# Optimization experiments

Measured on AMD Instinct MI355X. Metric: run time of the kernel, lower is better.

The kernel has to match this reference:

```python
import jax, jax.numpy as jnp
import numpy as np

D_MODEL = 1024
N_HEADS = 16
N_KV_HEADS = 4
HEAD_DIM = 64


def setup_inputs() -> dict:
    key = jax.random.key(0)
    ks = jax.random.split(key, 5)
    B, T, P = 2, 512, 8
    scale = 1.0 / np.sqrt(D_MODEL)
    return {
        "hidden_states": jax.random.normal(ks[0], (B, T, P, D_MODEL), dtype=jnp.float32),
        # weights stored [in, out] so y = x @ W (same math as nn.Linear with W^T)
        "Wq": jax.random.normal(ks[1], (D_MODEL, N_HEADS * HEAD_DIM), dtype=jnp.float32) * scale,
        "Wk": jax.random.normal(ks[2], (D_MODEL, N_KV_HEADS * HEAD_DIM), dtype=jnp.float32) * scale,
        "Wv": jax.random.normal(ks[3], (D_MODEL, N_KV_HEADS * HEAD_DIM), dtype=jnp.float32) * scale,
        "Wo": jax.random.normal(ks[4], (N_HEADS * HEAD_DIM, D_MODEL), dtype=jnp.float32) * scale,
    }


def _rope_tables(T, d):
    half = d // 2
    inv_freq = 1.0 / (10000.0 ** (jnp.arange(half, dtype=jnp.float32) / half))
    pos = jnp.arange(T, dtype=jnp.float32)
    angles = pos[:, None] * inv_freq[None, :]  # (T, half)
    return jnp.cos(angles), jnp.sin(angles)


def _apply_rope(x, cos, sin):
    # x: (B, P, T, H, d); cos/sin: (T, d/2)
    half = x.shape[-1] // 2
    x1, x2 = x[..., :half], x[..., half:]
    c = cos[None, None, :, None, :]
    s = sin[None, None, :, None, :]
    return jnp.concatenate([x1 * c - x2 * s, x1 * s + x2 * c], axis=-1)


def reference(hidden_states, Wq, Wk, Wv, Wo):
    B, T, P, _ = hidden_states.shape
    x = jnp.transpose(hidden_states, (0, 2, 1, 3))  # (B, P, T, C)
    q = (x @ Wq).reshape(B, P, T, N_HEADS, HEAD_DIM)
    k = (x @ Wk).reshape(B, P, T, N_KV_HEADS, HEAD_DIM)
    v = (x @ Wv).reshape(B, P, T, N_KV_HEADS, HEAD_DIM)

    rep = N_HEADS // N_KV_HEADS
    k = jnp.repeat(k, rep, axis=3)  # (B,P,T,H,d) interleaved like torch repeat/view
    v = jnp.repeat(v, rep, axis=3)

    cos, sin = _rope_tables(T, HEAD_DIM)
    q = _apply_rope(q, cos, sin)
    k = _apply_rope(k, cos, sin)

    # (B,P,H,T,d)
    q = jnp.transpose(q, (0, 1, 3, 2, 4))
    k = jnp.transpose(k, (0, 1, 3, 2, 4))
    v = jnp.transpose(v, (0, 1, 3, 2, 4))

    attn = jnp.einsum("bphqd,bphkd->bphqk", q, k) / jnp.sqrt(
        jnp.asarray(HEAD_DIM, q.dtype))
    attn = jax.nn.softmax(attn, axis=-1)
    out = jnp.einsum("bphqk,bphkd->bphqd", attn, v)
    out = jnp.transpose(out, (0, 1, 3, 2, 4)).reshape(B, P, T, N_HEADS * HEAD_DIM)
    out = jnp.transpose(out, (0, 2, 1, 3))  # (B, T, P, H*d)
    return out @ Wo
```

## Files before the change

### kernel.cpp

```cpp
#include <hip/hip_runtime.h>
#include <stdint.h>


typedef __attribute__((ext_vector_type(8))) short bf16x8;
typedef __attribute__((ext_vector_type(4))) float f32x4;
typedef __attribute__((ext_vector_type(16))) float f32x16;
typedef __attribute__((ext_vector_type(4))) unsigned short us4;
typedef __attribute__((ext_vector_type(8))) unsigned short us8;

static __device__ __forceinline__ unsigned short f2bf(float f) {
  unsigned u = __float_as_uint(f);
  u += 0x7fffu + ((u >> 16) & 1u);
  return (unsigned short)(u >> 16);
}

static __device__ __forceinline__ void ld_lds16(const void* g, void* l) {
  __builtin_amdgcn_global_load_lds(
      (const __attribute__((address_space(1))) void*)g,
      (__attribute__((address_space(3))) void*)l, 16, 0, 0);
}

static __device__ __forceinline__ f32x4 mfma16(bf16x8 a, bf16x8 b, f32x4 c) {
  return __builtin_amdgcn_mfma_f32_16x16x32_bf16(a, b, c, 0, 0, 0);
}
static __device__ __forceinline__ f32x16 mfma32(bf16x8 a, bf16x8 b, f32x16 c) {
  return __builtin_amdgcn_mfma_f32_32x32x16_bf16(a, b, c, 0, 0, 0);
}

__global__ __launch_bounds__(256) void conv_all(
    const float* __restrict__ hs, const float* __restrict__ Wq,
    const float* __restrict__ Wk, const float* __restrict__ Wv,
    const float* __restrict__ Wo, unsigned short* __restrict__ xb,
    unsigned short* __restrict__ wqkv, unsigned short* __restrict__ wot) {
  __shared__ float tile[64][65];
  int bid = blockIdx.x, tid = threadIdx.x;
  if (bid < 8192) {
    int gid = bid * 256 + tid;
    size_t e = (size_t)gid * 4;
    int r = (int)(e >> 10);
    int d = (int)(e & 1023);
    int b = r >> 12, p = (r >> 9) & 7, t = r & 511;
    const float4* src = (const float4*)(hs + ((((size_t)b * 512 + t) * 8 + p) << 10) + d);
    float4 v = *src;
    us4 o;
    o.x = f2bf(v.x); o.y = f2bf(v.y); o.z = f2bf(v.z); o.w = f2bf(v.w);
    *(us4*)(xb + e) = o;
    return;
  }
  int tb = bid - 8192;
  const float* W; unsigned short* Wt; int N, tc0, tn0;
  if (tb < 256)      { W = Wq; Wt = wqkv;                       N = 1024; tc0 = (tb >> 4) * 64;          tn0 = (tb & 15) * 64; }
  else if (tb < 320) { W = Wk; Wt = wqkv + (size_t)1024 * 1024; N = 256;  tc0 = ((tb - 256) >> 2) * 64;  tn0 = ((tb - 256) & 3) * 64; }
  else if (tb < 384) { W = Wv; Wt = wqkv + (size_t)1280 * 1024; N = 256;  tc0 = ((tb - 320) >> 2) * 64;  tn0 = ((tb - 320) & 3) * 64; }
  else               { W = Wo; Wt = wot;                        N = 1024; tc0 = ((tb - 384) >> 4) * 64;  tn0 = ((tb - 384) & 15) * 64; }
  int tr = tid >> 4, tc = tid & 15;
#pragma unroll
  for (int i = 0; i < 4; ++i) {
    int c = tr + i * 16;
    float4 v = *(const float4*)(W + (size_t)(tc0 + c) * N + tn0 + tc * 4);
    tile[c][tc * 4 + 0] = v.x; tile[c][tc * 4 + 1] = v.y;
    tile[c][tc * 4 + 2] = v.z; tile[c][tc * 4 + 3] = v.w;
  }
  __syncthreads();
#pragma unroll
  for (int i = 0; i < 4; ++i) {
    int n = tr + i * 16;
    us4 o;
    o.x = f2bf(tile[tc * 4 + 0][n]); o.y = f2bf(tile[tc * 4 + 1][n]);
    o.z = f2bf(tile[tc * 4 + 2][n]); o.w = f2bf(tile[tc * 4 + 3][n]);
    *(us4*)(Wt + (size_t)(tn0 + n) * 1024 + tc0 + tc * 4) = o;
  }
}

template <int NT, int MODE>
__global__ __launch_bounds__(256, 3) void gemm_bt(
    const unsigned short* __restrict__ A, const unsigned short* __restrict__ Bt,
    unsigned short* __restrict__ qb, unsigned short* __restrict__ kb,
    unsigned short* __restrict__ vtb, float* __restrict__ out) {
  constexpr int K = 1024;
  __shared__ __align__(16) unsigned short Sm[128 * 128];
  unsigned short* As = Sm;
  unsigned short* Bs = Sm + 128 * 64;
  unsigned short* Cs = Sm;

  int tid = threadIdx.x;
  int lane = tid & 63, wid = tid >> 6;
  int quad = lane >> 4, lo = lane & 15;
  int tn = blockIdx.x % NT, tm = blockIdx.x / NT;
  int wm = (wid >> 1) * 64, wn = (wid & 1) * 64;
  int srow = lane >> 3, schunk = lane & 7;

  f32x4 z = {0.f, 0.f, 0.f, 0.f};
  f32x4 acc[4][4];
  for (int i = 0; i < 4; ++i) for (int j = 0; j < 4; ++j) acc[i][j] = z;

  int cg = schunk ^ srow;
  const unsigned short* pa = A + ((size_t)(tm * 128) + wid * 8 + srow) * K + cg * 8;
  const unsigned short* pb = Bt + ((size_t)(tn * 128) + wid * 8 + srow) * K + cg * 8;
  char* dA = (char*)As + (wid * 8) * 128;
  char* dB = (char*)Bs + (wid * 8) * 128;

  for (int k0 = 0; k0 < K; k0 += 64) {
    __syncthreads();
#pragma unroll
    for (int i = 0; i < 4; ++i) {
      ld_lds16(pa + (size_t)i * 32 * K + k0, dA + i * 32 * 128);
      ld_lds16(pb + (size_t)i * 32 * K + k0, dB + i * 32 * 128);
    }
    __syncthreads();
#pragma unroll
    for (int kk = 0; kk < 64; kk += 32) {
      bf16x8 af[4], bb[4];
#pragma unroll
      for (int mi = 0; mi < 4; ++mi) {
        int row = wm + mi * 16 + lo;
        int cgx = (quad + (kk >> 3)) ^ (row & 7);
        af[mi] = *(const bf16x8*)(As + (size_t)row * 64 + cgx * 8);
      }
#pragma unroll
      for (int ni = 0; ni < 4; ++ni) {
        int row = wn + ni * 16 + lo;
        int cgx = (quad + (kk >> 3)) ^ (row & 7);
        bb[ni] = *(const bf16x8*)(Bs + (size_t)row * 64 + cgx * 8);
      }
#pragma unroll
      for (int mi = 0; mi < 4; ++mi)
#pragma unroll
        for (int ni = 0; ni < 4; ++ni)
          acc[mi][ni] = mfma16(af[mi], bb[ni], acc[mi][ni]);
    }
  }

  __syncthreads();

  if (MODE == 0 && tn < 10) {
    float qscale = (tn < 8) ? 0.125f : 1.0f;
#pragma unroll
    for (int mi = 0; mi < 4; ++mi)
#pragma unroll
      for (int r = 0; r < 4; ++r) {
        int t = (tm * 128 + wm + mi * 16 + quad * 4 + r) & 511;
#pragma unroll
        for (int ni = 0; ni < 2; ++ni) {
          float inv = exp2f((float)(ni * 16 + lo) * -0.41524101186092029f);
          float ang = (float)t * inv;
          float s, c;
          __sincosf(ang, &s, &c);
          float x1 = acc[mi][ni][r], x2 = acc[mi][ni + 2][r];
          acc[mi][ni][r]     = (x1 * c - x2 * s) * qscale;
          acc[mi][ni + 2][r] = (x1 * s + x2 * c) * qscale;
        }
      }
#pragma unroll
    for (int mi = 0; mi < 4; ++mi)
#pragma unroll
      for (int ni = 0; ni < 4; ++ni)
#pragma unroll
        for (int r = 0; r < 4; ++r) {
          int row = wm + mi * 16 + quad * 4 + r;
          int col = wn + ni * 16 + lo;
          int cs = col ^ (((row >> 2) & 3) << 3);
          Cs[row * 128 + cs] = f2bf(acc[mi][ni][r]);
        }
    __syncthreads();
    int tc = tid & 15, ro = tid >> 4;
#pragma unroll
    for (int it = 0; it < 8; ++it) {
      int row = ro + 16 * it;
      int cs = (tc * 8) ^ (((row >> 2) & 3) << 3);
      us8 v = *(const us8*)(Cs + row * 128 + cs);
      size_t grow = (size_t)(tm * 128 + row);
      if (tn < 8) {
        *(us8*)(qb + grow * 1024 + tn * 128 + tc * 8) = v;
      } else {
        *(us8*)(kb + grow * 256 + (tn - 8) * 128 + tc * 8) = v;
      }
    }
  } else if (MODE == 0) {
#pragma unroll
    for (int mi = 0; mi < 4; ++mi)
#pragma unroll
      for (int ni = 0; ni < 4; ++ni)
#pragma unroll
        for (int r = 0; r < 4; ++r) {
          int trow = wm + mi * 16 + quad * 4 + r;
          int col = wn + ni * 16 + lo;
          Cs[col * 128 + (trow ^ ((col & 7) << 3))] = f2bf(acc[mi][ni][r]);
        }
    __syncthreads();
    int chunk = tid & 15, colIdx = tid >> 4;
    int bp = tm >> 2, tbase = (tm & 3) * 128;
#pragma unroll
    for (int it = 0; it < 8; ++it) {
      int col = colIdx + it * 16;
      int t0 = chunk * 8;
      us8 v = *(const us8*)(Cs + col * 128 + (t0 ^ ((col & 7) << 3)));
      int gc = (tn - 10) * 128 + col;
      int hh = gc >> 6, dd = gc & 63;
      *(us8*)(vtb + (((size_t)(bp * 4 + hh)) * 64 + dd) * 512 + tbase + t0) = v;
    }
  } else {
    for (int mi = 0; mi < 4; ++mi) {
      for (int ni = 0; ni < 4; ++ni) {
        int col = tn * 128 + wn + ni * 16 + lo;
        for (int r = 0; r < 4; ++r) {
          int grow = tm * 128 + wm + mi * 16 + quad * 4 + r;
          int bp = grow >> 9, t = grow & 511;
          int b = bp >> 3, p = bp & 7;
          out[((((size_t)b * 512 + t) * 8 + p) << 10) + col] = acc[mi][ni][r];
        }
      }
    }
  }
}

__global__ __launch_bounds__(256, 4) void attn(
    const unsigned short* __restrict__ qb, const unsigned short* __restrict__ kb,
    const unsigned short* __restrict__ vtb, unsigned short* __restrict__ ao) {
  __shared__ __align__(16) unsigned short Qs[128 * 64];
  __shared__ __align__(16) unsigned short Ks[64 * 64];
  __shared__ __align__(16) unsigned short Vs[64 * 64];

  int tid = threadIdx.x;
  int lane = tid & 63, wid = tid >> 6;
  int lo32 = lane & 31, hl = lane >> 5;
  int qt = blockIdx.x & 3, bph = blockIdx.x >> 2;
  int head = bph & 15, bp = bph >> 4;
  int kvh = head >> 2;
  int t0 = qt * 128;
  int srow = lane >> 3, schunk = lane & 7;

  const unsigned short* qg = qb + ((size_t)(bp * 512 + t0)) * 1024 + head * 64;
  const unsigned short* kg = kb + ((size_t)bp * 512) * 256 + kvh * 64;
  const unsigned short* vg = vtb + ((size_t)(bp * 4 + kvh)) * 64 * 512;

  for (int i = 0; i < 4; ++i) {
    int row = wid * 8 + i * 32 + srow;
    int cg = schunk ^ (row & 7);
    ld_lds16(qg + (size_t)row * 1024 + cg * 8, (char*)Qs + (wid * 8 + i * 32) * 128);
  }

  f32x16 z16 = {0.f};
  f32x16 o0 = z16, o1 = z16;
  float psum = 0.f;
  int qrow = wid * 32 + lo32;

  for (int kt = 0; kt < 512; kt += 64) {
    __syncthreads();
    for (int i = 0; i < 2; ++i) {
      int row = wid * 8 + i * 32 + srow;
      int cg = schunk ^ (row & 7);
      ld_lds16(kg + (size_t)(kt + row) * 256 + cg * 8, (char*)Ks + (wid * 8 + i * 32) * 128);
      ld_lds16(vg + (size_t)row * 512 + kt + cg * 8, (char*)Vs + (wid * 8 + i * 32) * 128);
    }
    __syncthreads();

    f32x16 st0 = z16, st1 = z16;
#pragma unroll
    for (int kkc = 0; kkc < 4; ++kkc) {
      int ch = 2 * kkc + hl;
      bf16x8 qf = *(const bf16x8*)(Qs + (size_t)qrow * 64 + ((ch ^ (qrow & 7)) * 8));
      bf16x8 kf0 = *(const bf16x8*)(Ks + (size_t)lo32 * 64 + ((ch ^ (lo32 & 7)) * 8));
      bf16x8 kf1 = *(const bf16x8*)(Ks + (size_t)(32 + lo32) * 64 + ((ch ^ (lo32 & 7)) * 8));
      st0 = mfma32(kf0, qf, st0);
      st1 = mfma32(kf1, qf, st1);
    }

#pragma unroll
    for (int t = 0; t < 2; ++t) {
      const f32x16& stv = t ? st1 : st0;
      unsigned pk[8], xpk[8];
#pragma unroll
      for (int p = 0; p < 8; ++p) {
        float e0 = __expf(stv[2 * p]);
        float e1 = __expf(stv[2 * p + 1]);
        psum += e0 + e1;
        pk[p] = ((__float_as_uint(e0) + 0x8000u) >> 16) |
                ((__float_as_uint(e1) + 0x8000u) & 0xffff0000u);
      }
#pragma unroll
      for (int p = 0; p < 8; ++p) xpk[p] = (unsigned)__shfl_xor((int)pk[p], 32);
#pragma unroll
      for (int cc = 0; cc < 2; ++cc) {
        int o = cc * 4;
        union { unsigned u[4]; bf16x8 v; } af;
        if (hl == 0) {
          af.u[0] = pk[o];      af.u[1] = pk[o + 1];
          af.u[2] = xpk[o];     af.u[3] = xpk[o + 1];
        } else {
          af.u[0] = xpk[o + 2]; af.u[1] = xpk[o + 3];
          af.u[2] = pk[o + 2];  af.u[3] = pk[o + 3];
        }
        int vch = 2 * (t * 2 + cc) + hl;
        bf16x8 v0 = *(const bf16x8*)(Vs + (size_t)lo32 * 64 + ((vch ^ (lo32 & 7)) * 8));
        bf16x8 v1 = *(const bf16x8*)(Vs + (size_t)(32 + lo32) * 64 + ((vch ^ (lo32 & 7)) * 8));
        o0 = mfma32(af.v, v0, o0);
        o1 = mfma32(af.v, v1, o1);
      }
    }
  }

  psum += __shfl_xor(psum, 32);
  float inv = 1.f / psum;
#pragma unroll
  for (int r = 0; r < 16; ++r) {
    int q_r = (r & 3) + 8 * (r >> 2) + 4 * hl;
    float sc = __shfl(inv, q_r);
    size_t grow = (size_t)(bp * 512 + t0 + wid * 32 + q_r);
    ao[grow * 1024 + head * 64 + lo32]      = f2bf(o0[r] * sc);
    ao[grow * 1024 + head * 64 + 32 + lo32] = f2bf(o1[r] * sc);
  }
}

extern "C" void kernel_launch(void* const* d_in, const int* in_sizes, int n_in,
                              void* d_out, int out_size, void* d_ws, size_t ws_size,
                              hipStream_t stream) {
  const float* hs = (const float*)d_in[0];
  const float* Wq = (const float*)d_in[1];
  const float* Wk = (const float*)d_in[2];
  const float* Wv = (const float*)d_in[3];
  const float* Wo = (const float*)d_in[4];
  float* out = (float*)d_out;

  unsigned short* xb   = (unsigned short*)d_ws;
  unsigned short* wqkv = xb + (size_t)8192 * 1024;
  unsigned short* wot  = wqkv + (size_t)1536 * 1024;
  unsigned short* qbuf = wot + (size_t)1024 * 1024;
  unsigned short* kbuf = qbuf + (size_t)8192 * 1024;
  unsigned short* vtb  = kbuf + (size_t)8192 * 256;
  unsigned short* ao   = xb;

  conv_all<<<8832, 256, 0, stream>>>(hs, Wq, Wk, Wv, Wo, xb, wqkv, wot);
  gemm_bt<12, 0><<<768, 256, 0, stream>>>(xb, wqkv, qbuf, kbuf, vtb, nullptr);
  attn<<<1024, 256, 0, stream>>>(qbuf, kbuf, vtb, ao);
  gemm_bt<8, 1><<<512, 256, 0, stream>>>(ao, wot, nullptr, nullptr, nullptr, out);
}
```

Baseline: 189.4 us.

## Replace 128x128 GEMM with double-buffered 256x256 eight-wave pipelined GEMM

Both projection GEMMs move from 128x128 tiles with 4 waves and a single LDS buffer to 256x256 tiles with 8 waves. The new kernel double-buffers LDS with async global-to-LDS prefetch two K-steps ahead, interleaves LDS fragment reads with MFMA phases using raw s_barrier and s_waitcnt, and raises wave priority around the MFMA bursts. This is meant to hide load latency and raise per-tile data reuse. The cost is far fewer blocks (192 and 128 on a 256-CU part), which leaves many CUs idle, plus higher register and LDS pressure.

```diff
diff --git a/kernel.cpp b/kernel.cpp
--- a/kernel.cpp
+++ b/kernel.cpp
@@ -73,77 +73,151 @@
 }
 
 template <int NT, int MODE>
-__global__ __launch_bounds__(256, 3) void gemm_bt(
+__global__ __launch_bounds__(512, 2) void gemm256(
     const unsigned short* __restrict__ A, const unsigned short* __restrict__ Bt,
     unsigned short* __restrict__ qb, unsigned short* __restrict__ kb,
     unsigned short* __restrict__ vtb, float* __restrict__ out) {
   constexpr int K = 1024;
-  __shared__ __align__(16) unsigned short Sm[128 * 128];
-  unsigned short* As = Sm;
-  unsigned short* Bs = Sm + 128 * 64;
-  unsigned short* Cs = Sm;
+  constexpr int KT = K / 64;
+  __shared__ __align__(16) unsigned short Sm[2][2][256 * 64];
+  unsigned short* Cs = &Sm[0][0][0];
 
   int tid = threadIdx.x;
   int lane = tid & 63, wid = tid >> 6;
   int quad = lane >> 4, lo = lane & 15;
   int tn = blockIdx.x % NT, tm = blockIdx.x / NT;
-  int wm = (wid >> 1) * 64, wn = (wid & 1) * 64;
+  int wr = wid >> 2, wc = wid & 3;
   int srow = lane >> 3, schunk = lane & 7;
+  int cg = schunk ^ srow;
+
+  const unsigned short* pa = A + ((size_t)(tm * 256) + wid * 8 + srow) * K + cg * 8;
+  const unsigned short* pb = Bt + ((size_t)(tn * 256) + wid * 8 + srow) * K + cg * 8;
 
   f32x4 z = {0.f, 0.f, 0.f, 0.f};
-  f32x4 acc[4][4];
-  for (int i = 0; i < 4; ++i) for (int j = 0; j < 4; ++j) acc[i][j] = z;
-
-  int cg = schunk ^ srow;
-  const unsigned short* pa = A + ((size_t)(tm * 128) + wid * 8 + srow) * K + cg * 8;
-  const unsigned short* pb = Bt + ((size_t)(tn * 128) + wid * 8 + srow) * K + cg * 8;
-  char* dA = (char*)As + (wid * 8) * 128;
-  char* dB = (char*)Bs + (wid * 8) * 128;
-
-  for (int k0 = 0; k0 < K; k0 += 64) {
-    __syncthreads();
+  f32x4 acc[8][4];
+#pragma unroll
+  for (int i = 0; i < 8; ++i)
+#pragma unroll
+    for (int j = 0; j < 4; ++j) acc[i][j] = z;
+
+  auto stage = [&](int t, int p) {
 #pragma unroll
     for (int i = 0; i < 4; ++i) {
-      ld_lds16(pa + (size_t)i * 32 * K + k0, dA + i * 32 * 128);
-      ld_lds16(pb + (size_t)i * 32 * K + k0, dB + i * 32 * 128);
-    }
-    __syncthreads();
-#pragma unroll
-    for (int kk = 0; kk < 64; kk += 32) {
-      bf16x8 af[4], bb[4];
-#pragma unroll
-      for (int mi = 0; mi < 4; ++mi) {
-        int row = wm + mi * 16 + lo;
-        int cgx = (quad + (kk >> 3)) ^ (row & 7);
-        af[mi] = *(const bf16x8*)(As + (size_t)row * 64 + cgx * 8);
-      }
-#pragma unroll
-      for (int ni = 0; ni < 4; ++ni) {
-        int row = wn + ni * 16 + lo;
-        int cgx = (quad + (kk >> 3)) ^ (row & 7);
-        bb[ni] = *(const bf16x8*)(Bs + (size_t)row * 64 + cgx * 8);
-      }
+      ld_lds16(pa + (size_t)i * 64 * K + t * 64,
+               (char*)&Sm[p][0][0] + (wid * 8 + i * 64) * 128);
+      ld_lds16(pb + (size_t)i * 64 * K + t * 64,
+               (char*)&Sm[p][1][0] + (wid * 8 + i * 64) * 128);
+    }
+  };
+
+  stage(0, 0);
+  stage(1, 1);
+  asm volatile("s_waitcnt vmcnt(8)" ::: "memory");
+  asm volatile("s_barrier" ::: "memory");
+
+  bf16x8 af[4][2], bb0[2][2], bb1[2][2];
+
+  for (int t = 0; t < KT; ++t) {
+    int p = t & 1;
+    const unsigned short* As = &Sm[p][0][0];
+    const unsigned short* Bs = &Sm[p][1][0];
+
+#pragma unroll
+    for (int mi = 0; mi < 4; ++mi)
+#pragma unroll
+      for (int kx = 0; kx < 2; ++kx) {
+        int row = wr * 128 + mi * 16 + lo;
+        int cgx = (quad + kx * 4) ^ (row & 7);
+        af[mi][kx] = *(const bf16x8*)(As + (size_t)row * 64 + cgx * 8);
+      }
+#pragma unroll
+    for (int ni = 0; ni < 2; ++ni)
+#pragma unroll
+      for (int kx = 0; kx < 2; ++kx) {
+        int row = wc * 64 + ni * 16 + lo;
+        int cgx = (quad + kx * 4) ^ (row & 7);
+        bb0[ni][kx] = *(const bf16x8*)(Bs + (size_t)row * 64 + cgx * 8);
+      }
+    asm volatile("s_barrier" ::: "memory");
+    __builtin_amdgcn_s_setprio(1);
+#pragma unroll
+    for (int kx = 0; kx < 2; ++kx)
 #pragma unroll
       for (int mi = 0; mi < 4; ++mi)
 #pragma unroll
-        for (int ni = 0; ni < 4; ++ni)
-          acc[mi][ni] = mfma16(af[mi], bb[ni], acc[mi][ni]);
-    }
-  }
-
-  __syncthreads();
-
-  if (MODE == 0 && tn < 10) {
-    float qscale = (tn < 8) ? 0.125f : 1.0f;
+        for (int ni = 0; ni < 2; ++ni)
+          acc[mi][ni] = mfma16(af[mi][kx], bb0[ni][kx], acc[mi][ni]);
+    __builtin_amdgcn_s_setprio(0);
+    asm volatile("s_barrier" ::: "memory");
+
+#pragma unroll
+    for (int ni = 0; ni < 2; ++ni)
+#pragma unroll
+      for (int kx = 0; kx < 2; ++kx) {
+        int row = wc * 64 + (ni + 2) * 16 + lo;
+        int cgx = (quad + kx * 4) ^ (row & 7);
+        bb1[ni][kx] = *(const bf16x8*)(Bs + (size_t)row * 64 + cgx * 8);
+      }
+    asm volatile("s_barrier" ::: "memory");
+    __builtin_amdgcn_s_setprio(1);
+#pragma unroll
+    for (int kx = 0; kx < 2; ++kx)
+#pragma unroll
+      for (int mi = 0; mi < 4; ++mi)
+#pragma unroll
+        for (int ni = 0; ni < 2; ++ni)
+          acc[mi][ni + 2] = mfma16(af[mi][kx], bb1[ni][kx], acc[mi][ni + 2]);
+    __builtin_amdgcn_s_setprio(0);
+    asm volatile("s_barrier" ::: "memory");
+
 #pragma unroll
     for (int mi = 0; mi < 4; ++mi)
 #pragma unroll
+      for (int kx = 0; kx < 2; ++kx) {
+        int row = wr * 128 + 64 + mi * 16 + lo;
+        int cgx = (quad + kx * 4) ^ (row & 7);
+        af[mi][kx] = *(const bf16x8*)(As + (size_t)row * 64 + cgx * 8);
+      }
+    asm volatile("s_barrier" ::: "memory");
+    __builtin_amdgcn_s_setprio(1);
+#pragma unroll
+    for (int kx = 0; kx < 2; ++kx)
+#pragma unroll
+      for (int mi = 0; mi < 4; ++mi)
+#pragma unroll
+        for (int ni = 0; ni < 2; ++ni)
+          acc[mi + 4][ni + 2] = mfma16(af[mi][kx], bb1[ni][kx], acc[mi + 4][ni + 2]);
+    __builtin_amdgcn_s_setprio(0);
+    asm volatile("s_barrier" ::: "memory");
+
+    bool pf = (t + 2 < KT);
+    if (pf) stage(t + 2, p);
+    __builtin_amdgcn_s_setprio(1);
+#pragma unroll
+    for (int kx = 0; kx < 2; ++kx)
+#pragma unroll
+      for (int mi = 0; mi < 4; ++mi)
+#pragma unroll
+        for (int ni = 0; ni < 2; ++ni)
+          acc[mi + 4][ni] = mfma16(af[mi][kx], bb0[ni][kx], acc[mi + 4][ni]);
+    __builtin_amdgcn_s_setprio(0);
+    if (pf) asm volatile("s_waitcnt vmcnt(8)" ::: "memory");
+    else    asm volatile("s_waitcnt vmcnt(0)" ::: "memory");
+    asm volatile("s_barrier" ::: "memory");
+  }
+
+  if (MODE == 0 && tn < 5) {
+    float qscale = (tn < 4) ? 0.125f : 1.0f;
+#pragma unroll
+    for (int mi = 0; mi < 8; ++mi)
+#pragma unroll
       for (int r = 0; r < 4; ++r) {
-        int t = (tm * 128 + wm + mi * 16 + quad * 4 + r) & 511;
+        int row = wr * 128 + mi * 16 + quad * 4 + r;
+        int tpos = (tm * 256 + row) & 511;
 #pragma unroll
         for (int ni = 0; ni < 2; ++ni) {
-          float inv = exp2f((float)(ni * 16 + lo) * -0.41524101186092029f);
-          float ang = (float)t * inv;
+          float invf = exp2f((float)(ni * 16 + lo) * -0.41524101186092029f);
+          float ang = (float)tpos * invf;
           float s, c;
           __sincosf(ang, &s, &c);
           float x1 = acc[mi][ni][r], x2 = acc[mi][ni + 2][r];
@@ -152,62 +226,58 @@
         }
       }
 #pragma unroll
-    for (int mi = 0; mi < 4; ++mi)
+    for (int mi = 0; mi < 8; ++mi)
 #pragma unroll
       for (int ni = 0; ni < 4; ++ni)
 #pragma unroll
         for (int r = 0; r < 4; ++r) {
-          int row = wm + mi * 16 + quad * 4 + r;
-          int col = wn + ni * 16 + lo;
+          int row = wr * 128 + mi * 16 + quad * 4 + r;
+          int col = wc * 64 + ni * 16 + lo;
           int cs = col ^ (((row >> 2) & 3) << 3);
-          Cs[row * 128 + cs] = f2bf(acc[mi][ni][r]);
+          Cs[row * 256 + cs] = f2bf(acc[mi][ni][r]);
         }
     __syncthreads();
-    int tc = tid & 15, ro = tid >> 4;
-#pragma unroll
-    for (int it = 0; it < 8; ++it) {
+    int tc = tid & 31, ro = tid >> 5;
+#pragma unroll
+    for (int it = 0; it < 16; ++it) {
       int row = ro + 16 * it;
       int cs = (tc * 8) ^ (((row >> 2) & 3) << 3);
-      us8 v = *(const us8*)(Cs + row * 128 + cs);
-      size_t grow = (size_t)(tm * 128 + row);
-      if (tn < 8) {
-        *(us8*)(qb + grow * 1024 + tn * 128 + tc * 8) = v;
-      } else {
-        *(us8*)(kb + grow * 256 + (tn - 8) * 128 + tc * 8) = v;
-      }
+      us8 v = *(const us8*)(Cs + row * 256 + cs);
+      size_t grow = (size_t)(tm * 256 + row);
+      if (tn < 4) *(us8*)(qb + grow * 1024 + tn * 256 + tc * 8) = v;
+      else        *(us8*)(kb + grow * 256 + tc * 8) = v;
     }
   } else if (MODE == 0) {
 #pragma unroll
-    for (int mi = 0; mi < 4; ++mi)
+    for (int mi = 0; mi < 8; ++mi)
 #pragma unroll
       for (int ni = 0; ni < 4; ++ni)
 #pragma unroll
         for (int r = 0; r < 4; ++r) {
-          int trow = wm + mi * 16 + quad * 4 + r;
-          int col = wn + ni * 16 + lo;
-          Cs[col * 128 + (trow ^ ((col & 7) << 3))] = f2bf(acc[mi][ni][r]);
+          int trow = wr * 128 + mi * 16 + quad * 4 + r;
+          int col = wc * 64 + ni * 16 + lo;
+          Cs[col * 256 + (trow ^ ((col & 7) << 3))] = f2bf(acc[mi][ni][r]);
         }
     __syncthreads();
-    int chunk = tid & 15, colIdx = tid >> 4;
-    int bp = tm >> 2, tbase = (tm & 3) * 128;
-#pragma unroll
-    for (int it = 0; it < 8; ++it) {
+    int t0 = (tid & 31) * 8, colIdx = tid >> 5;
+    int bp = tm >> 1, tbase = (tm & 1) * 256;
+#pragma unroll
+    for (int it = 0; it < 16; ++it) {
       int col = colIdx + it * 16;
-      int t0 = chunk * 8;
-      us8 v = *(const us8*)(Cs + col * 128 + (t0 ^ ((col & 7) << 3)));
-      int gc = (tn - 10) * 128 + col;
-      int hh = gc >> 6, dd = gc & 63;
+      us8 v = *(const us8*)(Cs + col * 256 + (t0 ^ ((col & 7) << 3)));
+      int hh = col >> 6, dd = col & 63;
       *(us8*)(vtb + (((size_t)(bp * 4 + hh)) * 64 + dd) * 512 + tbase + t0) = v;
     }
   } else {
-    for (int mi = 0; mi < 4; ++mi) {
+#pragma unroll
+    for (int mi = 0; mi < 8; ++mi) {
       for (int ni = 0; ni < 4; ++ni) {
-        int col = tn * 128 + wn + ni * 16 + lo;
+        int col = tn * 256 + wc * 64 + ni * 16 + lo;
         for (int r = 0; r < 4; ++r) {
-          int grow = tm * 128 + wm + mi * 16 + quad * 4 + r;
-          int bp = grow >> 9, t = grow & 511;
-          int b = bp >> 3, p = bp & 7;
-          out[((((size_t)b * 512 + t) * 8 + p) << 10) + col] = acc[mi][ni][r];
+          int grow = tm * 256 + wr * 128 + mi * 16 + quad * 4 + r;
+          int bp = grow >> 9, tt = grow & 511;
+          int b = bp >> 3, pp = bp & 7;
+          out[((((size_t)b * 512 + tt) * 8 + pp) << 10) + col] = acc[mi][ni][r];
         }
       }
     }
@@ -331,7 +401,7 @@
   unsigned short* ao   = xb;
 
   conv_all<<<8832, 256, 0, stream>>>(hs, Wq, Wk, Wv, Wo, xb, wqkv, wot);
-  gemm_bt<12, 0><<<768, 256, 0, stream>>>(xb, wqkv, qbuf, kbuf, vtb, nullptr);
+  gemm256<6, 0><<<192, 512, 0, stream>>>(xb, wqkv, qbuf, kbuf, vtb, nullptr);
   attn<<<1024, 256, 0, stream>>>(qbuf, kbuf, vtb, ao);
-  gemm_bt<8, 1><<<512, 256, 0, stream>>>(ao, wot, nullptr, nullptr, nullptr, out);
-}
+  gemm256<4, 1><<<128, 512, 0, stream>>>(ao, wot, nullptr, nullptr, nullptr, out);
+}
```

New measurement: 191.8 us. Within noise of the previous version (+1.3%).
